# Optimization experiments

Measured on AMD Instinct MI355X. Metric: run time of the kernel, lower is better.

Reference implementation:

```python
import jax, jax.numpy as jnp
import numpy as np

B, L, EMB, H, NL, E, MAXA, PAD = 64, 512, 400, 256, 3, 512, 32, 0


def setup_inputs() -> dict:
    key = jax.random.key(0)
    ks = jax.random.split(key, 12)
    s = lambda k, shape: jax.random.normal(k, shape, jnp.float32) * 0.02
    Semb = jax.random.normal(ks[0], (B, EMB, L), jnp.float32)
    word_ids = jax.random.randint(ks[1], (B, L), 0, 30000)
    y1 = jax.random.randint(ks[2], (B,), 0, L - MAXA)
    span = jax.random.randint(ks[3], (B,), 0, MAXA)
    y2 = y1 + span
    edges = jax.random.randint(ks[4], (B, E, 2), 0, L)
    return dict(
        Semb=Semb,
        ans_sent_word_ids=word_ids,
        y1_in_sent=y1,
        y2_in_sent=y2,
        edges=edges,
        W1=s(ks[5], (H, EMB)),                 # Initialized_Conv1d (k=1, no bias)
        hw_lin_W=s(ks[6], (2, H, H)), hw_lin_b=jnp.zeros((2, H), jnp.float32),
        hw_gate_W=s(ks[7], (2, H, H)), hw_gate_b=jnp.zeros((2, H), jnp.float32),
        gcn_W=s(ks[8], (NL, H, H)), gcn_b=jnp.zeros((NL, H), jnp.float32),
        conv_W=s(ks[9], (1, NL * H)), conv_b=jnp.zeros((1,), jnp.float32),
        lin_W=s(ks[10], (L, L)), lin_b=jnp.zeros((L,), jnp.float32),
    )


def reference(Semb, ans_sent_word_ids, y1_in_sent, y2_in_sent, edges,
              W1, hw_lin_W, hw_lin_b, hw_gate_W, hw_gate_b,
              gcn_W, gcn_b, conv_W, conv_b, lin_W, lin_b):
    # 1x1 conv: [B, EMB, L] -> [B, H, L]
    x = jnp.einsum('oi,bit->bot', W1, Semb)
    # 2-layer Highway (dropout is identity in eval)
    for i in range(2):
        gate = jax.nn.sigmoid(jnp.einsum('oi,bit->bot', hw_gate_W[i], x) + hw_gate_b[i][None, :, None])
        nonlin = jnp.einsum('oi,bit->bot', hw_lin_W[i], x) + hw_lin_b[i][None, :, None]
        x = gate * nonlin + (1.0 - gate) * x
    maskS = (ans_sent_word_ids != PAD).astype(x.dtype)            # [B, L]
    # answer-span mask (Aemb itself is dead code in the original forward's output)
    pos = y1_in_sent[:, None] + jnp.arange(MAXA)                   # [B, MAXA]
    maskA = (pos <= y2_in_sent[:, None]).astype(x.dtype)
    # dense adjacency from edge list (undirected since gcn_directed=False)
    bidx = jnp.broadcast_to(jnp.arange(B)[:, None], (B, E))
    adj = jnp.zeros((B, L, L), x.dtype)
    adj = adj.at[bidx, edges[..., 0], edges[..., 1]].set(1.0)
    adj = adj.at[bidx, edges[..., 1], edges[..., 0]].set(1.0)
    # GCN (C-GCN style: W(Ax) + W(x), note bias counted twice, /(deg+1), relu)
    h = x.transpose(0, 2, 1)                                       # [B, L, H]
    denom = jnp.sum(adj, axis=2, keepdims=True) + 1.0              # [B, L, 1]
    outs = []
    for l in range(NL):
        Ax = jnp.einsum('bls,bsh->blh', adj, h)
        AxW = jnp.einsum('blh,oh->blo', Ax + h, gcn_W[l]) + 2.0 * gcn_b[l]
        h = jax.nn.relu(AxW / denom)
        outs.append(h)
    cat = jnp.concatenate(outs, axis=2)                            # [B, L, NL*H]
    y = jax.nn.relu(jnp.einsum('blc,oc->bol', cat, conv_W) + conv_b[None, :, None])  # [B,1,L]
    logits = (jnp.einsum('bol,ml->bom', y, lin_W) + lin_b).squeeze(1)                # [B,L]
    logits = logits * maskS + (1.0 - maskS) * (-1e30)
    return (logits, maskA)
```

## Files before the change

### kernel.cpp

```cpp
#include <hip/hip_runtime.h>
#include <cstdint>

#define B 64
#define L 512
#define EMB 400
#define KPAD 416
#define H 256
#define NL 3
#define NE 512
#define MAXA 32
#define M_TOT (B * L)

typedef unsigned short u16;
typedef float f32x4 __attribute__((ext_vector_type(4)));
typedef short short8 __attribute__((ext_vector_type(8)));
typedef u16 u16x8 __attribute__((ext_vector_type(8)));

__device__ __forceinline__ float b2f(u16 u) {
  unsigned v = ((unsigned)u) << 16;
  return __builtin_bit_cast(float, v);
}
__device__ __forceinline__ u16 f2b(float f) {
  unsigned u = __builtin_bit_cast(unsigned, f);
  unsigned r = (u + 0x7fffu + ((u >> 16) & 1u)) >> 16;
  return (u16)r;
}

#define GL16(g, l)                                                              \
  __builtin_amdgcn_global_load_lds((const __attribute__((address_space(1))) void*)(g), \
                                   (__attribute__((address_space(3))) void*)(l), 16, 0, 0)

template <int EPI>
__global__ __launch_bounds__(256, 2) void gemm64(
    const u16* __restrict__ A, const u16* __restrict__ Bw, const u16* __restrict__ B2w,
    const int K,
    const float* __restrict__ bias1, const float* __restrict__ bias2,
    const float* __restrict__ rden, const float* __restrict__ cw,
    float* __restrict__ yv, u16* __restrict__ Out) {
  constexpr bool HW = (EPI == 1);
  __shared__ u16 Bl0[256 * 32];
  __shared__ u16 Bl1[256 * 32];
  __shared__ u16 Al0[64 * 32];
  __shared__ u16 Al1[64 * 32];
  __shared__ u16 Cl0[HW ? 256 * 32 : 8];
  __shared__ u16 Cl1[HW ? 256 * 32 : 8];

  const int t = threadIdx.x;
  const int wid = t >> 6, lane = t & 63;
  const int m0 = blockIdx.x * 64;
  const int fr = lane & 15, kg = lane >> 4;
  const int r4 = t >> 2, ksg = t & 3;

  f32x4 acc[4][4] = {};
  f32x4 acc2[4][4] = {};

  auto stage = [&](u16* Ab, u16* Bb, u16* Cb, int kk) {
    const int kc = kk * 32 + ksg * 8;
#pragma unroll
    for (int c = 0; c < 4; ++c)
      GL16(Bw + (size_t)(c * 64 + r4) * K + kc, Bb + (size_t)(c * 256 + wid * 64) * 8);
    if constexpr (HW) {
#pragma unroll
      for (int c = 0; c < 4; ++c)
        GL16(B2w + (size_t)(c * 64 + r4) * K + kc, Cb + (size_t)(c * 256 + wid * 64) * 8);
    }
    GL16(A + (size_t)(m0 + r4) * K + kc, Ab + (size_t)(wid * 64) * 8);
  };
  auto compute = [&](const u16* Ab, const u16* Bb, const u16* Cb) {
    short8 af[4], bf[4], cf[4];
#pragma unroll
    for (int i = 0; i < 4; ++i) {
      af[i] = *(const short8*)(Ab + ((size_t)(i * 16 + fr) * 4 + kg) * 8);
      bf[i] = *(const short8*)(Bb + ((size_t)(wid * 64 + i * 16 + fr) * 4 + kg) * 8);
      if constexpr (HW)
        cf[i] = *(const short8*)(Cb + ((size_t)(wid * 64 + i * 16 + fr) * 4 + kg) * 8);
    }
#pragma unroll
    for (int mi = 0; mi < 4; ++mi)
#pragma unroll
      for (int ni = 0; ni < 4; ++ni) {
        acc[mi][ni] = __builtin_amdgcn_mfma_f32_16x16x32_bf16(af[mi], bf[ni], acc[mi][ni], 0, 0, 0);
        if constexpr (HW)
          acc2[mi][ni] =
              __builtin_amdgcn_mfma_f32_16x16x32_bf16(af[mi], cf[ni], acc2[mi][ni], 0, 0, 0);
      }
  };

  const int nk = K >> 5;
  stage(Al0, Bl0, Cl0, 0);
  for (int kk = 0; kk < nk; ++kk) {
    u16* Ac = (kk & 1) ? Al1 : Al0;
    u16* Bc = (kk & 1) ? Bl1 : Bl0;
    u16* Cc = (kk & 1) ? Cl1 : Cl0;
    u16* An = (kk & 1) ? Al0 : Al1;
    u16* Bn = (kk & 1) ? Bl0 : Bl1;
    u16* Cn = (kk & 1) ? Cl0 : Cl1;
    if (kk + 1 < nk) {
      stage(An, Bn, Cn, kk + 1);
      if constexpr (HW)
        asm volatile("s_waitcnt vmcnt(9)" ::: "memory");
      else
        asm volatile("s_waitcnt vmcnt(5)" ::: "memory");
    } else {
      asm volatile("s_waitcnt vmcnt(0)" ::: "memory");
    }
    __builtin_amdgcn_s_barrier();
    asm volatile("" ::: "memory");
    compute(Ac, Bc, Cc);
    __builtin_amdgcn_s_barrier();
    asm volatile("" ::: "memory");
  }

  const int r0 = kg * 4;
  const int c0 = wid * 64 + fr;
  if constexpr (EPI == 0) {
#pragma unroll
    for (int ni = 0; ni < 4; ++ni) {
      const int col = c0 + ni * 16;
#pragma unroll
      for (int mi = 0; mi < 4; ++mi)
#pragma unroll
        for (int rr = 0; rr < 4; ++rr)
          Out[(size_t)(m0 + mi * 16 + r0 + rr) * H + col] = f2b(acc[mi][ni][rr]);
    }
  } else if constexpr (EPI == 1) {
#pragma unroll
    for (int ni = 0; ni < 4; ++ni) {
      const int col = c0 + ni * 16;
      const float b1 = bias1[col], b2 = bias2[col];
#pragma unroll
      for (int mi = 0; mi < 4; ++mi)
#pragma unroll
        for (int rr = 0; rr < 4; ++rr) {
          const int row = m0 + mi * 16 + r0 + rr;
          const float g = 1.f / (1.f + __expf(-(acc[mi][ni][rr] + b1)));
          const float nn = acc2[mi][ni][rr] + b2;
          const float x = b2f(A[(size_t)row * K + col]);
          Out[(size_t)row * H + col] = f2b(g * nn + (1.f - g) * x);
        }
    }
  } else {
    float ypart[16];
#pragma unroll
    for (int q = 0; q < 16; ++q) ypart[q] = 0.f;
#pragma unroll
    for (int ni = 0; ni < 4; ++ni) {
      const int col = c0 + ni * 16;
      const float b1 = 2.f * bias1[col];
      const float cwv = cw[col];
#pragma unroll
      for (int mi = 0; mi < 4; ++mi)
#pragma unroll
        for (int rr = 0; rr < 4; ++rr) {
          const int row = m0 + mi * 16 + r0 + rr;
          const float s = (acc[mi][ni][rr] + b1) * rden[row];
          const float rl = s > 0.f ? s : 0.f;
          ypart[mi * 4 + rr] += rl * cwv;
          if constexpr (EPI == 2) Out[(size_t)row * H + col] = f2b(rl);
        }
    }
#pragma unroll
    for (int q = 0; q < 16; ++q) {
      float p = ypart[q];
      p += __shfl_xor(p, 1);
      p += __shfl_xor(p, 2);
      p += __shfl_xor(p, 4);
      p += __shfl_xor(p, 8);
      if (fr == 0) atomicAdd(&yv[m0 + (q >> 2) * 16 + r0 + (q & 3)], p);
    }
  }
}

__global__ __launch_bounds__(256) void k_gather(const unsigned* __restrict__ bm,
                                                const u16* __restrict__ h,
                                                u16* __restrict__ T) {
  const int t = threadIdx.x;
  const int tok = blockIdx.x * 8 + (t >> 5);
  const int b = tok >> 9;
  const int c = (t & 31) * 8;
  const uint4* wp4 = (const uint4*)(bm + (size_t)tok * 16);
  const uint4 w0 = wp4[0], w1 = wp4[1], w2 = wp4[2], w3 = wp4[3];
  const unsigned wa[16] = {w0.x, w0.y, w0.z, w0.w, w1.x, w1.y, w1.z, w1.w,
                           w2.x, w2.y, w2.z, w2.w, w3.x, w3.y, w3.z, w3.w};
  float acc[8];
  {
    const u16x8 v = *(const u16x8*)(h + (size_t)tok * H + c);
#pragma unroll
    for (int i = 0; i < 8; ++i) acc[i] = b2f(v[i]);
  }
#pragma unroll
  for (int wi = 0; wi < 16; ++wi) {
    unsigned bits = wa[wi];
    while (bits) {
      const int bit = __ffs(bits) - 1;
      bits &= bits - 1;
      const int s = wi * 32 + bit;
      const u16x8 u = *(const u16x8*)(h + (size_t)(b * L + s) * H + c);
#pragma unroll
      for (int i = 0; i < 8; ++i) acc[i] += b2f(u[i]);
    }
  }
  u16x8 o;
#pragma unroll
  for (int i = 0; i < 8; ++i) o[i] = f2b(acc[i]);
  *(u16x8*)(T + (size_t)tok * H + c) = o;
}

__global__ void k_edges(const int* __restrict__ edges, unsigned* __restrict__ bm) {
  const int t = blockIdx.x * 256 + threadIdx.x;
  const int b = t >> 9, e = t & 511;
  const int u = edges[(size_t)(b * NE + e) * 2 + 0];
  const int v = edges[(size_t)(b * NE + e) * 2 + 1];
  atomicOr(&bm[(size_t)(b * L + u) * 16 + (v >> 5)], 1u << (v & 31));
  atomicOr(&bm[(size_t)(b * L + v) * 16 + (u >> 5)], 1u << (u & 31));
}

#define NSEMBT (B * 56)
__global__ __launch_bounds__(256) void k_prep(const float* __restrict__ Semb,
                                              const float* __restrict__ W1,
                                              const float* __restrict__ gW,
                                              const float* __restrict__ lW,
                                              const float* __restrict__ gcnW,
                                              const unsigned* __restrict__ bm,
                                              u16* __restrict__ A0,
                                              u16* __restrict__ W1b, u16* __restrict__ HWGb,
                                              u16* __restrict__ HWLb, u16* __restrict__ GCNb,
                                              float* __restrict__ rden) {
  const int t = threadIdx.x;
  if (blockIdx.x < NSEMBT) {
    const int bid = blockIdx.x;
    const int b = bid / 56, rem = bid - b * 56;
    const int e0 = (rem >> 3) * 64, l0 = (rem & 7) * 64;
    __shared__ u16 tile[64][72];
    {
      const int er = t >> 2, ls = (t & 3) * 16;
      if (e0 + er < EMB) {
        const float* src = Semb + ((size_t)b * EMB + e0 + er) * L + l0 + ls;
#pragma unroll
        for (int i = 0; i < 4; ++i) {
          const float4 v = *(const float4*)(src + i * 4);
          tile[er][ls + i * 4 + 0] = f2b(v.x);
          tile[er][ls + i * 4 + 1] = f2b(v.y);
          tile[er][ls + i * 4 + 2] = f2b(v.z);
          tile[er][ls + i * 4 + 3] = f2b(v.w);
        }
      } else {
#pragma unroll
        for (int i = 0; i < 16; ++i) tile[er][ls + i] = 0;
      }
    }
    __syncthreads();
    {
      const int lr = t >> 2, es = (t & 3) * 16;
      if (e0 + es < KPAD) {
        u16x8 v0, v1;
#pragma unroll
        for (int i = 0; i < 8; ++i) v0[i] = tile[es + i][lr];
#pragma unroll
        for (int i = 0; i < 8; ++i) v1[i] = tile[es + 8 + i][lr];
        u16* dst = A0 + (size_t)(b * L + l0 + lr) * KPAD + e0 + es;
        *(u16x8*)dst = v0;
        *(u16x8*)(dst + 8) = v1;
      }
    }
    return;
  }
  int i = (blockIdx.x - NSEMBT) * 256 + t;
  if (i < 256 * KPAD) {
    const int o = i / KPAD, k = i - o * KPAD;
    W1b[i] = (k < EMB) ? f2b(W1[o * EMB + k]) : (u16)0;
    return;
  }
  i -= 256 * KPAD;
  if (i < 2 * H * H) { HWGb[i] = f2b(gW[i]); return; }
  i -= 2 * H * H;
  if (i < 2 * H * H) { HWLb[i] = f2b(lW[i]); return; }
  i -= 2 * H * H;
  if (i < NL * H * H) { GCNb[i] = f2b(gcnW[i]); return; }
  i -= NL * H * H;
  if (i < M_TOT) {
    const uint4* p = (const uint4*)(bm + (size_t)i * 16);
    int c = 0;
#pragma unroll
    for (int w = 0; w < 4; ++w) {
      const uint4 v = p[w];
      c += __popc(v.x) + __popc(v.y) + __popc(v.z) + __popc(v.w);
    }
    rden[i] = 1.f / (1.f + (float)c);
  }
}

__global__ __launch_bounds__(256) void k_logits(const float* __restrict__ yv,
                                                const float* __restrict__ cb,
                                                const float* __restrict__ lw,
                                                const float* __restrict__ lb,
                                                const int* __restrict__ wids,
                                                const int* __restrict__ y1,
                                                const int* __restrict__ y2,
                                                float* __restrict__ out) {
  if (blockIdx.x == B * 2) {
#pragma unroll
    for (int j = 0; j < 8; ++j) {
      const int idx = j * 256 + threadIdx.x;
      const int b = idx >> 5, q = idx & 31;
      out[B * L + idx] = (y1[b] + q <= y2[b]) ? 1.0f : 0.0f;
    }
    return;
  }
  const int b = blockIdx.x >> 1;
  const int m = ((blockIdx.x & 1) << 8) + threadIdx.x;
  __shared__ float ys[512];
  const float cb0 = cb[0];
  ys[threadIdx.x] = fmaxf(yv[(size_t)b * L + threadIdx.x] + cb0, 0.f);
  ys[threadIdx.x + 256] = fmaxf(yv[(size_t)b * L + 256 + threadIdx.x] + cb0, 0.f);
  __syncthreads();
  float acc = lb[m];
  const float4* wr = (const float4*)(lw + (size_t)m * L);
#pragma unroll 4
  for (int l4 = 0; l4 < 128; ++l4) {
    const float4 w4 = wr[l4];
    acc += ys[l4 * 4] * w4.x + ys[l4 * 4 + 1] * w4.y + ys[l4 * 4 + 2] * w4.z +
           ys[l4 * 4 + 3] * w4.w;
  }
  out[(size_t)b * L + m] = (wids[(size_t)b * L + m] != 0) ? acc : -1.0e30f;
}

extern "C" void kernel_launch(void* const* d_in, const int* in_sizes, int n_in,
                              void* d_out, int out_size, void* d_ws, size_t ws_size,
                              hipStream_t stream) {
  (void)in_sizes; (void)n_in; (void)out_size; (void)ws_size;
  const float* Semb      = (const float*)d_in[0];
  const int*   wids      = (const int*)d_in[1];
  const int*   y1        = (const int*)d_in[2];
  const int*   y2        = (const int*)d_in[3];
  const int*   edges     = (const int*)d_in[4];
  const float* W1        = (const float*)d_in[5];
  const float* hw_lin_W  = (const float*)d_in[6];
  const float* hw_lin_b  = (const float*)d_in[7];
  const float* hw_gate_W = (const float*)d_in[8];
  const float* hw_gate_b = (const float*)d_in[9];
  const float* gcn_W     = (const float*)d_in[10];
  const float* gcn_b     = (const float*)d_in[11];
  const float* conv_W    = (const float*)d_in[12];
  const float* conv_b    = (const float*)d_in[13];
  const float* lin_W     = (const float*)d_in[14];
  const float* lin_b     = (const float*)d_in[15];
  float* out = (float*)d_out;

  char* ws = (char*)d_ws;
  const size_t SZA = (size_t)M_TOT * KPAD * 2;
  const size_t SZX = (size_t)M_TOT * H * 2;
  u16* A0   = (u16*)(ws);
  u16* P0b  = (u16*)(ws + SZA);
  u16* P1b  = (u16*)(ws + SZA + SZX);
  u16* O0   = (u16*)(ws + SZA + 2 * SZX);
  u16* O1   = (u16*)(ws + SZA + 3 * SZX);
  char* wp  = ws + SZA + 4 * SZX;
  u16* W1b  = (u16*)(wp);
  u16* HWGb = (u16*)(wp + 212992);
  u16* HWLb = (u16*)(wp + 212992 + 262144);
  u16* GCNb = (u16*)(wp + 212992 + 2 * 262144);
  char* sp  = wp + 212992 + 2 * 262144 + 393216;
  unsigned* bm   = (unsigned*)(sp);
  float*    yv   = (float*)(sp + 2097152);
  float*    rden = (float*)(sp + 2097152 + 131072);

  hipMemsetAsync(bm, 0, 2097152 + 131072, stream);
  k_edges<<<dim3(B * NE / 256), 256, 0, stream>>>(edges, bm);

  const int ncvt = 256 * KPAD + 4 * H * H + NL * H * H + M_TOT;
  k_prep<<<dim3(NSEMBT + (ncvt + 255) / 256), 256, 0, stream>>>(
      Semb, W1, hw_gate_W, hw_lin_W, gcn_W, bm, A0, W1b, HWGb, HWLb, GCNb, rden);

  gemm64<0><<<dim3(M_TOT / 64), 256, 0, stream>>>(A0, W1b, nullptr, KPAD, nullptr, nullptr,
                                                  nullptr, nullptr, nullptr, P0b);
  gemm64<1><<<dim3(M_TOT / 64), 256, 0, stream>>>(P0b, HWGb, HWLb, H, hw_gate_b, hw_lin_b,
                                                  nullptr, nullptr, nullptr, P1b);
  gemm64<1><<<dim3(M_TOT / 64), 256, 0, stream>>>(P1b, HWGb + H * H, HWLb + H * H, H,
                                                  hw_gate_b + H, hw_lin_b + H, nullptr, nullptr,
                                                  nullptr, P0b);
  k_gather<<<dim3(M_TOT / 8), 256, 0, stream>>>(bm, P0b, P1b);
  gemm64<2><<<dim3(M_TOT / 64), 256, 0, stream>>>(P1b, GCNb, nullptr, H, gcn_b, nullptr,
                                                  rden, conv_W, yv, O0);
  k_gather<<<dim3(M_TOT / 8), 256, 0, stream>>>(bm, O0, P0b);
  gemm64<2><<<dim3(M_TOT / 64), 256, 0, stream>>>(P0b, GCNb + H * H, nullptr, H, gcn_b + H,
                                                  nullptr, rden, conv_W + H, yv, O1);
  k_gather<<<dim3(M_TOT / 8), 256, 0, stream>>>(bm, O1, P1b);
  gemm64<3><<<dim3(M_TOT / 64), 256, 0, stream>>>(P1b, GCNb + 2 * H * H, nullptr, H,
                                                  gcn_b + 2 * H, nullptr, rden,
                                                  conv_W + 2 * H, yv, nullptr);

  k_logits<<<dim3(B * 2 + 1), 256, 0, stream>>>(yv, conv_b, lin_W, lin_b, wids, y1, y2, out);
}
```

Baseline: 181.3 us.

## Fuse 1x1 conv and two highway layers into one kernel with LDS-resident activations

Replaces the three separate GEMM launches (conv projection and two highway layers) with one kernel that keeps each 64-row activation tile in shared memory across all three stages. This removes two global round-trips of the intermediate activations and two launches. The highway stages now load weights without double buffering, with full syncthreads around each k-step. The larger LDS footprint may reduce occupancy.

```diff
diff --git a/kernel.cpp b/kernel.cpp
--- a/kernel.cpp
+++ b/kernel.cpp
@@ -30,20 +30,16 @@
   __builtin_amdgcn_global_load_lds((const __attribute__((address_space(1))) void*)(g), \
                                    (__attribute__((address_space(3))) void*)(l), 16, 0, 0)
 
-template <int EPI>
-__global__ __launch_bounds__(256, 2) void gemm64(
-    const u16* __restrict__ A, const u16* __restrict__ Bw, const u16* __restrict__ B2w,
-    const int K,
-    const float* __restrict__ bias1, const float* __restrict__ bias2,
-    const float* __restrict__ rden, const float* __restrict__ cw,
-    float* __restrict__ yv, u16* __restrict__ Out) {
-  constexpr bool HW = (EPI == 1);
+__global__ __launch_bounds__(256, 2) void k_fused(
+    const u16* __restrict__ A0, const u16* __restrict__ W1b,
+    const u16* __restrict__ HWGb, const u16* __restrict__ HWLb,
+    const float* __restrict__ gbias, const float* __restrict__ lbias,
+    u16* __restrict__ Out) {
   __shared__ u16 Bl0[256 * 32];
   __shared__ u16 Bl1[256 * 32];
   __shared__ u16 Al0[64 * 32];
   __shared__ u16 Al1[64 * 32];
-  __shared__ u16 Cl0[HW ? 256 * 32 : 8];
-  __shared__ u16 Cl1[HW ? 256 * 32 : 8];
+  __shared__ u16 Xl[64 * 256];
 
   const int t = threadIdx.x;
   const int wid = t >> 6, lane = t & 63;
@@ -54,120 +50,214 @@
   f32x4 acc[4][4] = {};
   f32x4 acc2[4][4] = {};
 
-  auto stage = [&](u16* Ab, u16* Bb, u16* Cb, int kk) {
+  auto stage0 = [&](u16* Ab, u16* Bb, int kk) {
     const int kc = kk * 32 + ksg * 8;
 #pragma unroll
     for (int c = 0; c < 4; ++c)
-      GL16(Bw + (size_t)(c * 64 + r4) * K + kc, Bb + (size_t)(c * 256 + wid * 64) * 8);
-    if constexpr (HW) {
-#pragma unroll
-      for (int c = 0; c < 4; ++c)
-        GL16(B2w + (size_t)(c * 64 + r4) * K + kc, Cb + (size_t)(c * 256 + wid * 64) * 8);
-    }
-    GL16(A + (size_t)(m0 + r4) * K + kc, Ab + (size_t)(wid * 64) * 8);
+      GL16(W1b + (size_t)(c * 64 + r4) * KPAD + kc, Bb + (size_t)(c * 256 + wid * 64) * 8);
+    GL16(A0 + (size_t)(m0 + r4) * KPAD + kc, Ab + (size_t)(wid * 64) * 8);
   };
-  auto compute = [&](const u16* Ab, const u16* Bb, const u16* Cb) {
-    short8 af[4], bf[4], cf[4];
+  auto compute0 = [&](const u16* Ab, const u16* Bb) {
+    short8 af[4], bf[4];
 #pragma unroll
     for (int i = 0; i < 4; ++i) {
       af[i] = *(const short8*)(Ab + ((size_t)(i * 16 + fr) * 4 + kg) * 8);
       bf[i] = *(const short8*)(Bb + ((size_t)(wid * 64 + i * 16 + fr) * 4 + kg) * 8);
-      if constexpr (HW)
-        cf[i] = *(const short8*)(Cb + ((size_t)(wid * 64 + i * 16 + fr) * 4 + kg) * 8);
     }
 #pragma unroll
     for (int mi = 0; mi < 4; ++mi)
 #pragma unroll
-      for (int ni = 0; ni < 4; ++ni) {
+      for (int ni = 0; ni < 4; ++ni)
         acc[mi][ni] = __builtin_amdgcn_mfma_f32_16x16x32_bf16(af[mi], bf[ni], acc[mi][ni], 0, 0, 0);
-        if constexpr (HW)
-          acc2[mi][ni] =
-              __builtin_amdgcn_mfma_f32_16x16x32_bf16(af[mi], cf[ni], acc2[mi][ni], 0, 0, 0);
-      }
   };
+  {
+    const int nk = KPAD >> 5;
+    stage0(Al0, Bl0, 0);
+    for (int kk = 0; kk < nk; ++kk) {
+      u16* Ac = (kk & 1) ? Al1 : Al0;
+      u16* Bc = (kk & 1) ? Bl1 : Bl0;
+      u16* An = (kk & 1) ? Al0 : Al1;
+      u16* Bn = (kk & 1) ? Bl0 : Bl1;
+      if (kk + 1 < nk) {
+        stage0(An, Bn, kk + 1);
+        asm volatile("s_waitcnt vmcnt(5)" ::: "memory");
+      } else {
+        asm volatile("s_waitcnt vmcnt(0)" ::: "memory");
+      }
+      __builtin_amdgcn_s_barrier();
+      asm volatile("" ::: "memory");
+      compute0(Ac, Bc);
+      __builtin_amdgcn_s_barrier();
+      asm volatile("" ::: "memory");
+    }
+  }
+#pragma unroll
+  for (int ni = 0; ni < 4; ++ni) {
+    const int k = wid * 64 + ni * 16 + fr;
+    u16* xp = Xl + (size_t)(k >> 5) * 2048 + (k & 31);
+#pragma unroll
+    for (int mi = 0; mi < 4; ++mi)
+#pragma unroll
+      for (int rr = 0; rr < 4; ++rr)
+        xp[(size_t)(mi * 16 + kg * 4 + rr) * 32] = f2b(acc[mi][ni][rr]);
+  }
+  __syncthreads();
+
+  for (int layer = 0; layer < 2; ++layer) {
+    const u16* Gw = HWGb + layer * H * H;
+    const u16* Lw = HWLb + layer * H * H;
+#pragma unroll
+    for (int mi = 0; mi < 4; ++mi)
+#pragma unroll
+      for (int ni = 0; ni < 4; ++ni) { acc[mi][ni] = f32x4{}; acc2[mi][ni] = f32x4{}; }
+    for (int kk = 0; kk < 8; ++kk) {
+      const int kc = kk * 32 + ksg * 8;
+#pragma unroll
+      for (int c = 0; c < 4; ++c) {
+        GL16(Gw + (size_t)(c * 64 + r4) * H + kc, Bl0 + (size_t)(c * 256 + wid * 64) * 8);
+        GL16(Lw + (size_t)(c * 64 + r4) * H + kc, Bl1 + (size_t)(c * 256 + wid * 64) * 8);
+      }
+      __syncthreads();
+      short8 af[4], bf[4], cf[4];
+#pragma unroll
+      for (int i = 0; i < 4; ++i) {
+        af[i] = *(const short8*)(Xl + (size_t)kk * 2048 + (size_t)(i * 16 + fr) * 32 + kg * 8);
+        bf[i] = *(const short8*)(Bl0 + ((size_t)(wid * 64 + i * 16 + fr) * 4 + kg) * 8);
+        cf[i] = *(const short8*)(Bl1 + ((size_t)(wid * 64 + i * 16 + fr) * 4 + kg) * 8);
+      }
+#pragma unroll
+      for (int mi = 0; mi < 4; ++mi)
+#pragma unroll
+        for (int ni = 0; ni < 4; ++ni) {
+          acc[mi][ni] = __builtin_amdgcn_mfma_f32_16x16x32_bf16(af[mi], bf[ni], acc[mi][ni], 0, 0, 0);
+          acc2[mi][ni] = __builtin_amdgcn_mfma_f32_16x16x32_bf16(af[mi], cf[ni], acc2[mi][ni], 0, 0, 0);
+        }
+      __syncthreads();
+    }
+    u16 xres[64];
+#pragma unroll
+    for (int ni = 0; ni < 4; ++ni) {
+      const int col = wid * 64 + ni * 16 + fr;
+      const u16* xp = Xl + (size_t)(col >> 5) * 2048 + (col & 31);
+#pragma unroll
+      for (int mi = 0; mi < 4; ++mi)
+#pragma unroll
+        for (int rr = 0; rr < 4; ++rr)
+          xres[(ni * 4 + mi) * 4 + rr] = xp[(size_t)(mi * 16 + kg * 4 + rr) * 32];
+    }
+    __syncthreads();
+#pragma unroll
+    for (int ni = 0; ni < 4; ++ni) {
+      const int col = wid * 64 + ni * 16 + fr;
+      const float b1 = gbias[layer * H + col];
+      const float b2 = lbias[layer * H + col];
+      u16* xp = Xl + (size_t)(col >> 5) * 2048 + (col & 31);
+#pragma unroll
+      for (int mi = 0; mi < 4; ++mi)
+#pragma unroll
+        for (int rr = 0; rr < 4; ++rr) {
+          const float g = 1.f / (1.f + __expf(-(acc[mi][ni][rr] + b1)));
+          const float nn = acc2[mi][ni][rr] + b2;
+          const float x = b2f(xres[(ni * 4 + mi) * 4 + rr]);
+          const u16 v = f2b(g * nn + (1.f - g) * x);
+          if (layer == 0)
+            xp[(size_t)(mi * 16 + kg * 4 + rr) * 32] = v;
+          else
+            Out[(size_t)(m0 + mi * 16 + kg * 4 + rr) * H + col] = v;
+        }
+    }
+    __syncthreads();
+  }
+}
+
+template <int EPI>
+__global__ __launch_bounds__(256, 2) void gemm64(
+    const u16* __restrict__ A, const u16* __restrict__ Bw, const int K,
+    const float* __restrict__ bias1, const float* __restrict__ rden,
+    const float* __restrict__ cw, float* __restrict__ yv, u16* __restrict__ Out) {
+  __shared__ u16 Bl0[256 * 32];
+  __shared__ u16 Bl1[256 * 32];
+  __shared__ u16 Al0[64 * 32];
+  __shared__ u16 Al1[64 * 32];
+
+  const int t = threadIdx.x;
+  const int wid = t >> 6, lane = t & 63;
+  const int m0 = blockIdx.x * 64;
+  const int fr = lane & 15, kg = lane >> 4;
+  const int r4 = t >> 2, ksg = t & 3;
+
+  f32x4 acc[4][4] = {};
+
+  auto stage = [&](u16* Ab, u16* Bb, int kk) {
+    const int kc = kk * 32 + ksg * 8;
+#pragma unroll
+    for (int c = 0; c < 4; ++c)
+      GL16(Bw + (size_t)(c * 64 + r4) * K + kc, Bb + (size_t)(c * 256 + wid * 64) * 8);
+    GL16(A + (size_t)(m0 + r4) * K + kc, Ab + (size_t)(wid * 64) * 8);
+  };
+  auto compute = [&](const u16* Ab, const u16* Bb) {
+    short8 af[4], bf[4];
+#pragma unroll
+    for (int i = 0; i < 4; ++i) {
+      af[i] = *(const short8*)(Ab + ((size_t)(i * 16 + fr) * 4 + kg) * 8);
+      bf[i] = *(const short8*)(Bb + ((size_t)(wid * 64 + i * 16 + fr) * 4 + kg) * 8);
+    }
+#pragma unroll
+    for (int mi = 0; mi < 4; ++mi)
+#pragma unroll
+      for (int ni = 0; ni < 4; ++ni)
+        acc[mi][ni] = __builtin_amdgcn_mfma_f32_16x16x32_bf16(af[mi], bf[ni], acc[mi][ni], 0, 0, 0);
+  };
 
   const int nk = K >> 5;
-  stage(Al0, Bl0, Cl0, 0);
+  stage(Al0, Bl0, 0);
   for (int kk = 0; kk < nk; ++kk) {
     u16* Ac = (kk & 1) ? Al1 : Al0;
     u16* Bc = (kk & 1) ? Bl1 : Bl0;
-    u16* Cc = (kk & 1) ? Cl1 : Cl0;
     u16* An = (kk & 1) ? Al0 : Al1;
     u16* Bn = (kk & 1) ? Bl0 : Bl1;
-    u16* Cn = (kk & 1) ? Cl0 : Cl1;
     if (kk + 1 < nk) {
-      stage(An, Bn, Cn, kk + 1);
-      if constexpr (HW)
-        asm volatile("s_waitcnt vmcnt(9)" ::: "memory");
-      else
-        asm volatile("s_waitcnt vmcnt(5)" ::: "memory");
+      stage(An, Bn, kk + 1);
+      asm volatile("s_waitcnt vmcnt(5)" ::: "memory");
     } else {
       asm volatile("s_waitcnt vmcnt(0)" ::: "memory");
     }
     __builtin_amdgcn_s_barrier();
     asm volatile("" ::: "memory");
-    compute(Ac, Bc, Cc);
+    compute(Ac, Bc);
     __builtin_amdgcn_s_barrier();
     asm volatile("" ::: "memory");
   }
 
   const int r0 = kg * 4;
   const int c0 = wid * 64 + fr;
-  if constexpr (EPI == 0) {
-#pragma unroll
-    for (int ni = 0; ni < 4; ++ni) {
-      const int col = c0 + ni * 16;
-#pragma unroll
-      for (int mi = 0; mi < 4; ++mi)
-#pragma unroll
-        for (int rr = 0; rr < 4; ++rr)
-          Out[(size_t)(m0 + mi * 16 + r0 + rr) * H + col] = f2b(acc[mi][ni][rr]);
-    }
-  } else if constexpr (EPI == 1) {
-#pragma unroll
-    for (int ni = 0; ni < 4; ++ni) {
-      const int col = c0 + ni * 16;
-      const float b1 = bias1[col], b2 = bias2[col];
-#pragma unroll
-      for (int mi = 0; mi < 4; ++mi)
-#pragma unroll
-        for (int rr = 0; rr < 4; ++rr) {
-          const int row = m0 + mi * 16 + r0 + rr;
-          const float g = 1.f / (1.f + __expf(-(acc[mi][ni][rr] + b1)));
-          const float nn = acc2[mi][ni][rr] + b2;
-          const float x = b2f(A[(size_t)row * K + col]);
-          Out[(size_t)row * H + col] = f2b(g * nn + (1.f - g) * x);
-        }
-    }
-  } else {
-    float ypart[16];
-#pragma unroll
-    for (int q = 0; q < 16; ++q) ypart[q] = 0.f;
-#pragma unroll
-    for (int ni = 0; ni < 4; ++ni) {
-      const int col = c0 + ni * 16;
-      const float b1 = 2.f * bias1[col];
-      const float cwv = cw[col];
-#pragma unroll
-      for (int mi = 0; mi < 4; ++mi)
-#pragma unroll
-        for (int rr = 0; rr < 4; ++rr) {
-          const int row = m0 + mi * 16 + r0 + rr;
-          const float s = (acc[mi][ni][rr] + b1) * rden[row];
-          const float rl = s > 0.f ? s : 0.f;
-          ypart[mi * 4 + rr] += rl * cwv;
-          if constexpr (EPI == 2) Out[(size_t)row * H + col] = f2b(rl);
-        }
-    }
-#pragma unroll
-    for (int q = 0; q < 16; ++q) {
-      float p = ypart[q];
-      p += __shfl_xor(p, 1);
-      p += __shfl_xor(p, 2);
-      p += __shfl_xor(p, 4);
-      p += __shfl_xor(p, 8);
-      if (fr == 0) atomicAdd(&yv[m0 + (q >> 2) * 16 + r0 + (q & 3)], p);
-    }
+  float ypart[16];
+#pragma unroll
+  for (int q = 0; q < 16; ++q) ypart[q] = 0.f;
+#pragma unroll
+  for (int ni = 0; ni < 4; ++ni) {
+    const int col = c0 + ni * 16;
+    const float b1 = 2.f * bias1[col];
+    const float cwv = cw[col];
+#pragma unroll
+    for (int mi = 0; mi < 4; ++mi)
+#pragma unroll
+      for (int rr = 0; rr < 4; ++rr) {
+        const int row = m0 + mi * 16 + r0 + rr;
+        const float s = (acc[mi][ni][rr] + b1) * rden[row];
+        const float rl = s > 0.f ? s : 0.f;
+        ypart[mi * 4 + rr] += rl * cwv;
+        if constexpr (EPI == 2) Out[(size_t)row * H + col] = f2b(rl);
+      }
+  }
+#pragma unroll
+  for (int q = 0; q < 16; ++q) {
+    float p = ypart[q];
+    p += __shfl_xor(p, 1);
+    p += __shfl_xor(p, 2);
+    p += __shfl_xor(p, 4);
+    p += __shfl_xor(p, 8);
+    if (fr == 0) atomicAdd(&yv[m0 + (q >> 2) * 16 + r0 + (q & 3)], p);
   }
 }
 
@@ -372,22 +462,16 @@
   k_prep<<<dim3(NSEMBT + (ncvt + 255) / 256), 256, 0, stream>>>(
       Semb, W1, hw_gate_W, hw_lin_W, gcn_W, bm, A0, W1b, HWGb, HWLb, GCNb, rden);
 
-  gemm64<0><<<dim3(M_TOT / 64), 256, 0, stream>>>(A0, W1b, nullptr, KPAD, nullptr, nullptr,
-                                                  nullptr, nullptr, nullptr, P0b);
-  gemm64<1><<<dim3(M_TOT / 64), 256, 0, stream>>>(P0b, HWGb, HWLb, H, hw_gate_b, hw_lin_b,
-                                                  nullptr, nullptr, nullptr, P1b);
-  gemm64<1><<<dim3(M_TOT / 64), 256, 0, stream>>>(P1b, HWGb + H * H, HWLb + H * H, H,
-                                                  hw_gate_b + H, hw_lin_b + H, nullptr, nullptr,
-                                                  nullptr, P0b);
+  k_fused<<<dim3(M_TOT / 64), 256, 0, stream>>>(A0, W1b, HWGb, HWLb,
+                                                hw_gate_b, hw_lin_b, P0b);
+
   k_gather<<<dim3(M_TOT / 8), 256, 0, stream>>>(bm, P0b, P1b);
-  gemm64<2><<<dim3(M_TOT / 64), 256, 0, stream>>>(P1b, GCNb, nullptr, H, gcn_b, nullptr,
-                                                  rden, conv_W, yv, O0);
+  gemm64<2><<<dim3(M_TOT / 64), 256, 0, stream>>>(P1b, GCNb, H, gcn_b, rden, conv_W, yv, O0);
   k_gather<<<dim3(M_TOT / 8), 256, 0, stream>>>(bm, O0, P0b);
-  gemm64<2><<<dim3(M_TOT / 64), 256, 0, stream>>>(P0b, GCNb + H * H, nullptr, H, gcn_b + H,
-                                                  nullptr, rden, conv_W + H, yv, O1);
+  gemm64<2><<<dim3(M_TOT / 64), 256, 0, stream>>>(P0b, GCNb + H * H, H, gcn_b + H, rden,
+                                                  conv_W + H, yv, O1);
   k_gather<<<dim3(M_TOT / 8), 256, 0, stream>>>(bm, O1, P1b);
-  gemm64<3><<<dim3(M_TOT / 64), 256, 0, stream>>>(P1b, GCNb + 2 * H * H, nullptr, H,
-                                                  gcn_b + 2 * H, nullptr, rden,
+  gemm64<3><<<dim3(M_TOT / 64), 256, 0, stream>>>(P1b, GCNb + 2 * H * H, H, gcn_b + 2 * H, rden,
                                                   conv_W + 2 * H, yv, nullptr);
 
   k_logits<<<dim3(B * 2 + 1), 256, 0, stream>>>(yv, conv_b, lin_W, lin_b, wids, y1, y2, out);
```

Result: slower. 188.5 us (+3.9%).

## Switch GEMM and gather pipeline from bf16 to fp8 with permuted K layout

Applied to the files above, without the earlier changes.

Converts all activations and weights to fp8 e4m3 instead of bf16 and uses fp8 MFMA instructions with a 64-wide K tile. The K dimension is permuted so each lane's 16-byte load splits into two 8-byte MFMA operands. The intent is to halve memory traffic in the GEMMs and the adjacency gather, and to use the higher fp8 matrix throughput. The cost is a large loss of precision across five chained GEMMs and the GCN sums, which may break the accuracy tolerance. K padding grows from 416 to 448.

```diff
diff --git a/kernel.cpp b/kernel.cpp
--- a/kernel.cpp
+++ b/kernel.cpp
@@ -4,26 +4,45 @@
 #define B 64
 #define L 512
 #define EMB 400
-#define KPAD 416
+#define KPAD 448
 #define H 256
 #define NL 3
 #define NE 512
 #define MAXA 32
 #define M_TOT (B * L)
 
+typedef unsigned char u8;
 typedef unsigned short u16;
+typedef unsigned long long ull;
 typedef float f32x4 __attribute__((ext_vector_type(4)));
-typedef short short8 __attribute__((ext_vector_type(8)));
-typedef u16 u16x8 __attribute__((ext_vector_type(8)));
-
-__device__ __forceinline__ float b2f(u16 u) {
-  unsigned v = ((unsigned)u) << 16;
-  return __builtin_bit_cast(float, v);
-}
-__device__ __forceinline__ u16 f2b(float f) {
+typedef ull u64x2 __attribute__((ext_vector_type(2)));
+
+__device__ __forceinline__ int perm64(int k) {
+  return (k & ~63) | (((k >> 3) & 3) << 4) | (((k >> 5) & 1) << 3) | (k & 7);
+}
+
+__device__ __forceinline__ u8 f2fp8(float f) {
   unsigned u = __builtin_bit_cast(unsigned, f);
-  unsigned r = (u + 0x7fffu + ((u >> 16) & 1u)) >> 16;
-  return (u16)r;
+  const unsigned s = (u >> 31) << 7;
+  unsigned au = u & 0x7fffffffu;
+  if (au >= 0x43e00000u) return (u8)(s | 0x7e);
+  unsigned r = au + 0x7ffffu + ((au >> 20) & 1u);
+  if (r >= 0x3c800000u) {
+    unsigned e = (r >> 23) - 120u;
+    unsigned m = (r >> 20) & 7u;
+    return (u8)(s | (e << 3) | m);
+  }
+  float af = __builtin_bit_cast(float, au);
+  unsigned m = (unsigned)(af * 512.0f + 0.5f);
+  return (u8)(s | m);
+}
+
+__device__ __forceinline__ float fp8d(unsigned v) {
+  const unsigned e = (v >> 3) & 15, m = v & 7;
+  float f;
+  if (e == 0) f = (float)m * 0.001953125f;
+  else f = __builtin_bit_cast(float, ((e + 120u) << 23) | (m << 20));
+  return (v >> 7) ? -f : f;
 }
 
 #define GL16(g, l)                                                              \
@@ -32,18 +51,18 @@
 
 template <int EPI>
 __global__ __launch_bounds__(256, 2) void gemm64(
-    const u16* __restrict__ A, const u16* __restrict__ Bw, const u16* __restrict__ B2w,
+    const u8* __restrict__ A, const u8* __restrict__ Bw, const u8* __restrict__ B2w,
     const int K,
     const float* __restrict__ bias1, const float* __restrict__ bias2,
     const float* __restrict__ rden, const float* __restrict__ cw,
-    float* __restrict__ yv, u16* __restrict__ Out) {
+    float* __restrict__ yv, u8* __restrict__ Out) {
   constexpr bool HW = (EPI == 1);
-  __shared__ u16 Bl0[256 * 32];
-  __shared__ u16 Bl1[256 * 32];
-  __shared__ u16 Al0[64 * 32];
-  __shared__ u16 Al1[64 * 32];
-  __shared__ u16 Cl0[HW ? 256 * 32 : 8];
-  __shared__ u16 Cl1[HW ? 256 * 32 : 8];
+  __shared__ u8 Bl0[256 * 64];
+  __shared__ u8 Bl1[256 * 64];
+  __shared__ u8 Al0[64 * 64];
+  __shared__ u8 Al1[64 * 64];
+  __shared__ u8 Cl0[HW ? 256 * 64 : 16];
+  __shared__ u8 Cl1[HW ? 256 * 64 : 16];
 
   const int t = threadIdx.x;
   const int wid = t >> 6, lane = t & 63;
@@ -54,47 +73,53 @@
   f32x4 acc[4][4] = {};
   f32x4 acc2[4][4] = {};
 
-  auto stage = [&](u16* Ab, u16* Bb, u16* Cb, int kk) {
-    const int kc = kk * 32 + ksg * 8;
+  auto stage = [&](u8* Ab, u8* Bb, u8* Cb, int kk) {
+    const int kc = kk * 64 + ksg * 16;
 #pragma unroll
     for (int c = 0; c < 4; ++c)
-      GL16(Bw + (size_t)(c * 64 + r4) * K + kc, Bb + (size_t)(c * 256 + wid * 64) * 8);
+      GL16(Bw + (size_t)(c * 64 + r4) * K + kc, Bb + (size_t)(c * 256 + wid * 64) * 16);
     if constexpr (HW) {
 #pragma unroll
       for (int c = 0; c < 4; ++c)
-        GL16(B2w + (size_t)(c * 64 + r4) * K + kc, Cb + (size_t)(c * 256 + wid * 64) * 8);
-    }
-    GL16(A + (size_t)(m0 + r4) * K + kc, Ab + (size_t)(wid * 64) * 8);
+        GL16(B2w + (size_t)(c * 64 + r4) * K + kc, Cb + (size_t)(c * 256 + wid * 64) * 16);
+    }
+    GL16(A + (size_t)(m0 + r4) * K + kc, Ab + (size_t)(wid * 64) * 16);
   };
-  auto compute = [&](const u16* Ab, const u16* Bb, const u16* Cb) {
-    short8 af[4], bf[4], cf[4];
+  auto compute = [&](const u8* Ab, const u8* Bb, const u8* Cb) {
+    u64x2 af[4], bf[4], cf[4];
 #pragma unroll
     for (int i = 0; i < 4; ++i) {
-      af[i] = *(const short8*)(Ab + ((size_t)(i * 16 + fr) * 4 + kg) * 8);
-      bf[i] = *(const short8*)(Bb + ((size_t)(wid * 64 + i * 16 + fr) * 4 + kg) * 8);
+      af[i] = *(const u64x2*)(Ab + ((size_t)(i * 16 + fr) * 4 + kg) * 16);
+      bf[i] = *(const u64x2*)(Bb + ((size_t)(wid * 64 + i * 16 + fr) * 4 + kg) * 16);
       if constexpr (HW)
-        cf[i] = *(const short8*)(Cb + ((size_t)(wid * 64 + i * 16 + fr) * 4 + kg) * 8);
+        cf[i] = *(const u64x2*)(Cb + ((size_t)(wid * 64 + i * 16 + fr) * 4 + kg) * 16);
     }
 #pragma unroll
     for (int mi = 0; mi < 4; ++mi)
 #pragma unroll
       for (int ni = 0; ni < 4; ++ni) {
-        acc[mi][ni] = __builtin_amdgcn_mfma_f32_16x16x32_bf16(af[mi], bf[ni], acc[mi][ni], 0, 0, 0);
-        if constexpr (HW)
-          acc2[mi][ni] =
-              __builtin_amdgcn_mfma_f32_16x16x32_bf16(af[mi], cf[ni], acc2[mi][ni], 0, 0, 0);
+        acc[mi][ni] = __builtin_amdgcn_mfma_f32_16x16x32_fp8_fp8(af[mi][0], bf[ni][0],
+                                                                 acc[mi][ni], 0, 0, 0);
+        acc[mi][ni] = __builtin_amdgcn_mfma_f32_16x16x32_fp8_fp8(af[mi][1], bf[ni][1],
+                                                                 acc[mi][ni], 0, 0, 0);
+        if constexpr (HW) {
+          acc2[mi][ni] = __builtin_amdgcn_mfma_f32_16x16x32_fp8_fp8(af[mi][0], cf[ni][0],
+                                                                    acc2[mi][ni], 0, 0, 0);
+          acc2[mi][ni] = __builtin_amdgcn_mfma_f32_16x16x32_fp8_fp8(af[mi][1], cf[ni][1],
+                                                                    acc2[mi][ni], 0, 0, 0);
+        }
       }
   };
 
-  const int nk = K >> 5;
+  const int nk = K >> 6;
   stage(Al0, Bl0, Cl0, 0);
   for (int kk = 0; kk < nk; ++kk) {
-    u16* Ac = (kk & 1) ? Al1 : Al0;
-    u16* Bc = (kk & 1) ? Bl1 : Bl0;
-    u16* Cc = (kk & 1) ? Cl1 : Cl0;
-    u16* An = (kk & 1) ? Al0 : Al1;
-    u16* Bn = (kk & 1) ? Bl0 : Bl1;
-    u16* Cn = (kk & 1) ? Cl0 : Cl1;
+    u8* Ac = (kk & 1) ? Al1 : Al0;
+    u8* Bc = (kk & 1) ? Bl1 : Bl0;
+    u8* Cc = (kk & 1) ? Cl1 : Cl0;
+    u8* An = (kk & 1) ? Al0 : Al1;
+    u8* Bn = (kk & 1) ? Bl0 : Bl1;
+    u8* Cn = (kk & 1) ? Cl0 : Cl1;
     if (kk + 1 < nk) {
       stage(An, Bn, Cn, kk + 1);
       if constexpr (HW)
@@ -117,16 +142,18 @@
 #pragma unroll
     for (int ni = 0; ni < 4; ++ni) {
       const int col = c0 + ni * 16;
+      const int pc = perm64(col);
 #pragma unroll
       for (int mi = 0; mi < 4; ++mi)
 #pragma unroll
         for (int rr = 0; rr < 4; ++rr)
-          Out[(size_t)(m0 + mi * 16 + r0 + rr) * H + col] = f2b(acc[mi][ni][rr]);
+          Out[(size_t)(m0 + mi * 16 + r0 + rr) * H + pc] = f2fp8(acc[mi][ni][rr]);
     }
   } else if constexpr (EPI == 1) {
 #pragma unroll
     for (int ni = 0; ni < 4; ++ni) {
       const int col = c0 + ni * 16;
+      const int pc = perm64(col);
       const float b1 = bias1[col], b2 = bias2[col];
 #pragma unroll
       for (int mi = 0; mi < 4; ++mi)
@@ -135,8 +162,8 @@
           const int row = m0 + mi * 16 + r0 + rr;
           const float g = 1.f / (1.f + __expf(-(acc[mi][ni][rr] + b1)));
           const float nn = acc2[mi][ni][rr] + b2;
-          const float x = b2f(A[(size_t)row * K + col]);
-          Out[(size_t)row * H + col] = f2b(g * nn + (1.f - g) * x);
+          const float x = fp8d(A[(size_t)row * H + pc]);
+          Out[(size_t)row * H + pc] = f2fp8(g * nn + (1.f - g) * x);
         }
     }
   } else {
@@ -146,6 +173,7 @@
 #pragma unroll
     for (int ni = 0; ni < 4; ++ni) {
       const int col = c0 + ni * 16;
+      const int pc = perm64(col);
       const float b1 = 2.f * bias1[col];
       const float cwv = cw[col];
 #pragma unroll
@@ -156,7 +184,7 @@
           const float s = (acc[mi][ni][rr] + b1) * rden[row];
           const float rl = s > 0.f ? s : 0.f;
           ypart[mi * 4 + rr] += rl * cwv;
-          if constexpr (EPI == 2) Out[(size_t)row * H + col] = f2b(rl);
+          if constexpr (EPI == 2) Out[(size_t)row * H + pc] = f2fp8(rl);
         }
     }
 #pragma unroll
@@ -172,8 +200,8 @@
 }
 
 __global__ __launch_bounds__(256) void k_gather(const unsigned* __restrict__ bm,
-                                                const u16* __restrict__ h,
-                                                u16* __restrict__ T) {
+                                                const u8* __restrict__ h,
+                                                u8* __restrict__ T) {
   const int t = threadIdx.x;
   const int tok = blockIdx.x * 8 + (t >> 5);
   const int b = tok >> 9;
@@ -184,9 +212,9 @@
                            w2.x, w2.y, w2.z, w2.w, w3.x, w3.y, w3.z, w3.w};
   float acc[8];
   {
-    const u16x8 v = *(const u16x8*)(h + (size_t)tok * H + c);
-#pragma unroll
-    for (int i = 0; i < 8; ++i) acc[i] = b2f(v[i]);
+    const ull v = *(const ull*)(h + (size_t)tok * H + c);
+#pragma unroll
+    for (int i = 0; i < 8; ++i) acc[i] = fp8d((unsigned)(v >> (8 * i)) & 255u);
   }
 #pragma unroll
   for (int wi = 0; wi < 16; ++wi) {
@@ -195,15 +223,15 @@
       const int bit = __ffs(bits) - 1;
       bits &= bits - 1;
       const int s = wi * 32 + bit;
-      const u16x8 u = *(const u16x8*)(h + (size_t)(b * L + s) * H + c);
-#pragma unroll
-      for (int i = 0; i < 8; ++i) acc[i] += b2f(u[i]);
-    }
-  }
-  u16x8 o;
-#pragma unroll
-  for (int i = 0; i < 8; ++i) o[i] = f2b(acc[i]);
-  *(u16x8*)(T + (size_t)tok * H + c) = o;
+      const ull u = *(const ull*)(h + (size_t)(b * L + s) * H + c);
+#pragma unroll
+      for (int i = 0; i < 8; ++i) acc[i] += fp8d((unsigned)(u >> (8 * i)) & 255u);
+    }
+  }
+  ull o = 0;
+#pragma unroll
+  for (int i = 0; i < 8; ++i) o |= (ull)f2fp8(acc[i]) << (8 * i);
+  *(ull*)(T + (size_t)tok * H + c) = o;
 }
 
 __global__ void k_edges(const int* __restrict__ edges, unsigned* __restrict__ bm) {
@@ -222,16 +250,16 @@
                                               const float* __restrict__ lW,
                                               const float* __restrict__ gcnW,
                                               const unsigned* __restrict__ bm,
-                                              u16* __restrict__ A0,
-                                              u16* __restrict__ W1b, u16* __restrict__ HWGb,
-                                              u16* __restrict__ HWLb, u16* __restrict__ GCNb,
+                                              u8* __restrict__ A0,
+                                              u8* __restrict__ W1b, u8* __restrict__ HWGb,
+                                              u8* __restrict__ HWLb, u8* __restrict__ GCNb,
                                               float* __restrict__ rden) {
   const int t = threadIdx.x;
   if (blockIdx.x < NSEMBT) {
     const int bid = blockIdx.x;
     const int b = bid / 56, rem = bid - b * 56;
     const int e0 = (rem >> 3) * 64, l0 = (rem & 7) * 64;
-    __shared__ u16 tile[64][72];
+    __shared__ u8 tile[64][68];
     {
       const int er = t >> 2, ls = (t & 3) * 16;
       if (e0 + er < EMB) {
@@ -239,10 +267,10 @@
 #pragma unroll
         for (int i = 0; i < 4; ++i) {
           const float4 v = *(const float4*)(src + i * 4);
-          tile[er][ls + i * 4 + 0] = f2b(v.x);
-          tile[er][ls + i * 4 + 1] = f2b(v.y);
-          tile[er][ls + i * 4 + 2] = f2b(v.z);
-          tile[er][ls + i * 4 + 3] = f2b(v.w);
+          tile[er][ls + i * 4 + 0] = f2fp8(v.x);
+          tile[er][ls + i * 4 + 1] = f2fp8(v.y);
+          tile[er][ls + i * 4 + 2] = f2fp8(v.z);
+          tile[er][ls + i * 4 + 3] = f2fp8(v.w);
         }
       } else {
 #pragma unroll
@@ -252,31 +280,41 @@
     __syncthreads();
     {
       const int lr = t >> 2, es = (t & 3) * 16;
-      if (e0 + es < KPAD) {
-        u16x8 v0, v1;
-#pragma unroll
-        for (int i = 0; i < 8; ++i) v0[i] = tile[es + i][lr];
-#pragma unroll
-        for (int i = 0; i < 8; ++i) v1[i] = tile[es + 8 + i][lr];
-        u16* dst = A0 + (size_t)(b * L + l0 + lr) * KPAD + e0 + es;
-        *(u16x8*)dst = v0;
-        *(u16x8*)(dst + 8) = v1;
-      }
+      u8* dst = A0 + (size_t)(b * L + l0 + lr) * KPAD;
+      ull r0 = 0, r1 = 0;
+#pragma unroll
+      for (int i = 0; i < 8; ++i) r0 |= (ull)tile[es + i][lr] << (8 * i);
+#pragma unroll
+      for (int i = 0; i < 8; ++i) r1 |= (ull)tile[es + 8 + i][lr] << (8 * i);
+      *(ull*)(dst + perm64(e0 + es)) = r0;
+      *(ull*)(dst + perm64(e0 + es + 8)) = r1;
     }
     return;
   }
   int i = (blockIdx.x - NSEMBT) * 256 + t;
   if (i < 256 * KPAD) {
     const int o = i / KPAD, k = i - o * KPAD;
-    W1b[i] = (k < EMB) ? f2b(W1[o * EMB + k]) : (u16)0;
+    W1b[o * KPAD + perm64(k)] = (k < EMB) ? f2fp8(W1[o * EMB + k]) : (u8)0;
     return;
   }
   i -= 256 * KPAD;
-  if (i < 2 * H * H) { HWGb[i] = f2b(gW[i]); return; }
+  if (i < 2 * H * H) {
+    const int o = i >> 8, k = i & 255;
+    HWGb[o * H + perm64(k)] = f2fp8(gW[i]);
+    return;
+  }
   i -= 2 * H * H;
-  if (i < 2 * H * H) { HWLb[i] = f2b(lW[i]); return; }
+  if (i < 2 * H * H) {
+    const int o = i >> 8, k = i & 255;
+    HWLb[o * H + perm64(k)] = f2fp8(lW[i]);
+    return;
+  }
   i -= 2 * H * H;
-  if (i < NL * H * H) { GCNb[i] = f2b(gcnW[i]); return; }
+  if (i < NL * H * H) {
+    const int o = i >> 8, k = i & 255;
+    GCNb[o * H + perm64(k)] = f2fp8(gcnW[i]);
+    return;
+  }
   i -= NL * H * H;
   if (i < M_TOT) {
     const uint4* p = (const uint4*)(bm + (size_t)i * 16);
@@ -348,19 +386,19 @@
   float* out = (float*)d_out;
 
   char* ws = (char*)d_ws;
-  const size_t SZA = (size_t)M_TOT * KPAD * 2;
-  const size_t SZX = (size_t)M_TOT * H * 2;
-  u16* A0   = (u16*)(ws);
-  u16* P0b  = (u16*)(ws + SZA);
-  u16* P1b  = (u16*)(ws + SZA + SZX);
-  u16* O0   = (u16*)(ws + SZA + 2 * SZX);
-  u16* O1   = (u16*)(ws + SZA + 3 * SZX);
-  char* wp  = ws + SZA + 4 * SZX;
-  u16* W1b  = (u16*)(wp);
-  u16* HWGb = (u16*)(wp + 212992);
-  u16* HWLb = (u16*)(wp + 212992 + 262144);
-  u16* GCNb = (u16*)(wp + 212992 + 2 * 262144);
-  char* sp  = wp + 212992 + 2 * 262144 + 393216;
+  const size_t SZA = (size_t)M_TOT * KPAD;
+  const size_t SZX = (size_t)M_TOT * H;
+  u8* A0   = (u8*)(ws);
+  u8* P0b  = (u8*)(ws + SZA);
+  u8* P1b  = (u8*)(ws + SZA + SZX);
+  u8* O0   = (u8*)(ws + SZA + 2 * SZX);
+  u8* O1   = (u8*)(ws + SZA + 3 * SZX);
+  char* wp = ws + SZA + 4 * SZX;
+  u8* W1b  = (u8*)(wp);
+  u8* HWGb = (u8*)(wp + 114688);
+  u8* HWLb = (u8*)(wp + 114688 + 131072);
+  u8* GCNb = (u8*)(wp + 114688 + 2 * 131072);
+  char* sp = wp + 114688 + 2 * 131072 + 196608;
   unsigned* bm   = (unsigned*)(sp);
   float*    yv   = (float*)(sp + 2097152);
   float*    rden = (float*)(sp + 2097152 + 131072);
```

Result: slower. 229.6 us (+26.7%).
